# Optimization experiments

Hardware: AMD Instinct MI355X
Metric: run time of the kernel (lower is better)

Reference implementation:

```python
import jax, jax.numpy as jnp
import numpy as np

B, N_OP, N_MA, F, H, O = 32, 512, 64, 8, 128, 8


def _lin(k, fan_in, fan_out):
    kw, kb = jax.random.split(k)
    bound = 1.0 / np.sqrt(fan_in)
    w = jax.random.uniform(kw, (fan_in, fan_out), jnp.float32, -bound, bound)
    b = jax.random.uniform(kb, (fan_out,), jnp.float32, -bound, bound)
    return w, b


def setup_inputs() -> dict:
    key = jax.random.key(0)
    ks = jax.random.split(key, 12)
    inp = {
        "ope_ma_adj_batch": jax.random.randint(ks[0], (B, N_OP, N_MA), 0, 2, dtype=jnp.int32),
        "feats_op": jax.random.normal(ks[1], (B, N_OP, F), jnp.float32),
        "feats_ma": jax.random.normal(ks[2], (B, N_MA, F), jnp.float32),
    }
    # MLPsim 0 (machine aggregation): Linear(F,H), Linear(H,H), Linear(H,O)
    inp["l0_w1"], inp["l0_b1"] = _lin(ks[3], F, H)
    inp["l0_w2"], inp["l0_b2"] = _lin(ks[4], H, H)
    inp["l0_w3"], inp["l0_b3"] = _lin(ks[5], H, O)
    # MLPsim 1 (self-loop aggregation)
    inp["l1_w1"], inp["l1_b1"] = _lin(ks[6], F, H)
    inp["l1_w2"], inp["l1_b2"] = _lin(ks[7], H, H)
    inp["l1_w3"], inp["l1_b3"] = _lin(ks[8], H, O)
    # Final project: Linear(2*O,H), Linear(H,H), Linear(H,O)
    inp["p_w1"], inp["p_b1"] = _lin(ks[9], 2 * O, H)
    inp["p_w2"], inp["p_b2"] = _lin(ks[10], H, H)
    inp["p_w3"], inp["p_b3"] = _lin(ks[11], H, O)
    return inp


def _mlp3(x, w1, b1, w2, b2, w3, b3):
    # Linear -> ELU -> Linear -> ELU -> Linear (matches nn.Sequential in MLPsim.project)
    x = jax.nn.elu(x @ w1 + b1)
    x = jax.nn.elu(x @ w2 + b2)
    return x @ w3 + b3


def reference(ope_ma_adj_batch, feats_op, feats_ma,
              l0_w1, l0_b1, l0_w2, l0_b2, l0_w3, l0_b3,
              l1_w1, l1_b1, l1_w2, l1_b2, l1_w3, l1_b3,
              p_w1, p_b1, p_w2, p_b2, p_w3, p_b3):
    # MLPsim: adj.unsqueeze(-1)*feat.unsqueeze(-3) then sum(-2) == adj @ feat
    adj = ope_ma_adj_batch.astype(feats_ma.dtype)
    agg_ma = jnp.einsum('bnm,bmf->bnf', adj, feats_ma)       # (B, N_op, F)
    emb0 = _mlp3(agg_ma, l0_w1, l0_b1, l0_w2, l0_b2, l0_w3, l0_b3)
    # Second adjacency is the identity self-loop: I @ feats_op == feats_op
    emb1 = _mlp3(feats_op, l1_w1, l1_b1, l1_w2, l1_b2, l1_w3, l1_b3)
    cat = jnp.concatenate([emb0, emb1], axis=-1)              # (B, N_op, 2*O)
    # Final project: ELU -> Linear -> ELU -> Linear -> ELU -> Linear
    mu = _mlp3(jax.nn.elu(cat), p_w1, p_b1, p_w2, p_b2, p_w3, p_b3)
    return mu
```

## Files before the change

kernel.cpp:

```cpp
#include <hip/hip_runtime.h>

#define BB    32
#define N_OPC 512
#define N_MAC 64
#define FF    8
#define HH    128
#define OO    8
#define TM    32
#define ASTRB 136

typedef _Float16 f16x8 __attribute__((ext_vector_type(8)));
typedef _Float16 f16x4 __attribute__((ext_vector_type(4)));
typedef float    f32x4 __attribute__((ext_vector_type(4)));

__device__ __forceinline__ float elu_f(float x) {
    return x > 0.0f ? x : (__expf(x) - 1.0f);
}
__device__ __forceinline__ void store_f16(float v, ushort* dst, int off) {
    const _Float16 h = (_Float16)v;
    dst[off] = __builtin_bit_cast(ushort, h);
}
__device__ __forceinline__ f16x8 gather8(const float* __restrict__ w, int kbase, int j, int ld) {
    f16x8 v;
    #pragma unroll
    for (int i = 0; i < 8; ++i)
        v[i] = (_Float16)w[(kbase + i) * ld + j];
    return v;
}

__device__ __forceinline__ void epi_store(f32x4 a, const float* __restrict__ bias, int jb,
                                          ushort* __restrict__ dst, int off)
{
    const float4 bb = *(const float4*)(bias + jb);
    f16x4 v;
    v[0] = (_Float16)elu_f(a[0] + bb.x);
    v[1] = (_Float16)elu_f(a[1] + bb.y);
    v[2] = (_Float16)elu_f(a[2] + bb.z);
    v[3] = (_Float16)elu_f(a[3] + bb.w);
    *(f16x4*)(dst + off) = v;
}

__global__ __launch_bounds__(512, 4) void mlps_kernel(
    const int*   __restrict__ adj,
    const float* __restrict__ fop,
    const float* __restrict__ fmab,
    const float* __restrict__ l0w1, const float* __restrict__ l0b1,
    const float* __restrict__ l0w2, const float* __restrict__ l0b2,
    const float* __restrict__ l0w3, const float* __restrict__ l0b3,
    const float* __restrict__ l1w1, const float* __restrict__ l1b1,
    const float* __restrict__ l1w2, const float* __restrict__ l1b2,
    const float* __restrict__ l1w3, const float* __restrict__ l1b3,
    const float* __restrict__ pw1,  const float* __restrict__ pb1,
    const float* __restrict__ pw2,  const float* __restrict__ pb2,
    const float* __restrict__ pw3,  const float* __restrict__ pb3,
    float* __restrict__ out)
{
    __shared__ __align__(16) ushort hbuf[2][TM * ASTRB];
    __shared__ __align__(16) ushort gbuf[2][TM * ASTRB];
    __shared__ float fmS[N_MAC * FF];
    __shared__ __align__(16) ushort xinF[TM * FF];
    __shared__ __align__(16) ushort xopF[TM * FF];
    __shared__ __align__(16) ushort catF[TM * 16];

    const int tid  = threadIdx.x;
    const int wv   = tid >> 6;
    const int lane = tid & 63;
    const int lrow = lane & 15;
    const int lk   = lane >> 4;
    const int row0 = blockIdx.x * TM;
    const int b    = row0 / N_OPC;
    const int br   = wv >> 2, jt0 = (wv & 3) * 2;

    const float* w1p = br ? l1w1 : l0w1;
    f16x8 w1f[2] = {};
    if (lk == 0) {
        w1f[0] = gather8(w1p, 0, jt0 * 16 + lrow, HH);
        w1f[1] = gather8(w1p, 0, (jt0 + 1) * 16 + lrow, HH);
    }
    const float* w2p = br ? l1w2 : l0w2;
    f16x8 wf2[2][4];
    #pragma unroll
    for (int jtl = 0; jtl < 2; ++jtl)
        #pragma unroll
        for (int ks = 0; ks < 4; ++ks)
            wf2[jtl][ks] = gather8(w2p, ks * 32 + lk * 8, (jt0 + jtl) * 16 + lrow, HH);

    fmS[tid] = fmab[b * N_MAC * FF + tid];
    if (tid < TM * FF)
        store_f16(fop[row0 * FF + tid], xopF, tid);
    __syncthreads();

    if (tid < TM * FF) {
        const int r = tid >> 3, f = tid & 7;
        const int* arow = adj + (row0 + r) * N_MAC;
        float a = 0.0f;
        #pragma unroll
        for (int m4 = 0; m4 < N_MAC; m4 += 4) {
            const int4 av = *(const int4*)(arow + m4);
            a = fmaf((float)av.x, fmS[(m4 + 0) * FF + f], a);
            a = fmaf((float)av.y, fmS[(m4 + 1) * FF + f], a);
            a = fmaf((float)av.z, fmS[(m4 + 2) * FF + f], a);
            a = fmaf((float)av.w, fmS[(m4 + 3) * FF + f], a);
        }
        store_f16(a, xinF, tid);
    }
    __syncthreads();

    {
        const ushort* xF = br ? xopF : xinF;
        const float* b1 = br ? l1b1 : l0b1;
        f16x8 X[2] = {};
        if (lk == 0) {
            #pragma unroll
            for (int rt = 0; rt < 2; ++rt)
                X[rt] = *(const f16x8*)(xF + (rt * 16 + lrow) * 8);
        }
        f32x4 acc[2][2] = {};
        #pragma unroll
        for (int jtl = 0; jtl < 2; ++jtl)
            #pragma unroll
            for (int rt = 0; rt < 2; ++rt)
                acc[jtl][rt] = __builtin_amdgcn_mfma_f32_16x16x32_f16(w1f[jtl], X[rt], acc[jtl][rt], 0, 0, 0);
        #pragma unroll
        for (int jtl = 0; jtl < 2; ++jtl) {
            const int jb = (jt0 + jtl) * 16 + lk * 4;
            #pragma unroll
            for (int rt = 0; rt < 2; ++rt)
                epi_store(acc[jtl][rt], b1, jb, hbuf[br], (rt * 16 + lrow) * ASTRB + jb);
        }
    }
    __syncthreads();

    f16x8 wf3[4] = {};
    if (wv < 4 && lrow < OO) {
        const float* w3p = (wv >> 1) ? l1w3 : l0w3;
        #pragma unroll
        for (int ks = 0; ks < 4; ++ks)
            wf3[ks] = gather8(w3p, ks * 32 + lk * 8, lrow, OO);
    }
    {
        const ushort* aF = hbuf[br];
        f32x4 acc[2][2] = {};
        #pragma unroll
        for (int ks = 0; ks < 4; ++ks) {
            f16x8 x[2];
            #pragma unroll
            for (int rt = 0; rt < 2; ++rt)
                x[rt] = *(const f16x8*)(aF + (rt * 16 + lrow) * ASTRB + ks * 32 + lk * 8);
            #pragma unroll
            for (int jtl = 0; jtl < 2; ++jtl)
                #pragma unroll
                for (int rt = 0; rt < 2; ++rt)
                    acc[jtl][rt] = __builtin_amdgcn_mfma_f32_16x16x32_f16(wf2[jtl][ks], x[rt], acc[jtl][rt], 0, 0, 0);
        }
        const float* b2 = br ? l1b2 : l0b2;
        #pragma unroll
        for (int jtl = 0; jtl < 2; ++jtl) {
            const int jb = (jt0 + jtl) * 16 + lk * 4;
            #pragma unroll
            for (int rt = 0; rt < 2; ++rt)
                epi_store(acc[jtl][rt], b2, jb, gbuf[br], (rt * 16 + lrow) * ASTRB + jb);
        }
    }
    __syncthreads();

    f16x8 wf4 = {};
    if (lk < 2)
        wf4 = gather8(pw1, lk * 8, wv * 16 + lrow, HH);
    if (wv < 4) {
        const int br3 = wv >> 1, rt = wv & 1;
        const ushort* aF = gbuf[br3];
        f32x4 acc = {};
        #pragma unroll
        for (int ks = 0; ks < 4; ++ks) {
            const f16x8 x = *(const f16x8*)(aF + (rt * 16 + lrow) * ASTRB + ks * 32 + lk * 8);
            acc = __builtin_amdgcn_mfma_f32_16x16x32_f16(wf3[ks], x, acc, 0, 0, 0);
        }
        if (lk < 2) {
            const float* b3 = br3 ? l1b3 : l0b3;
            epi_store(acc, b3, lk * 4, catF, (rt * 16 + lrow) * 16 + br3 * OO + lk * 4);
        }
    }
    __syncthreads();

    f16x8 wf5[4];
    #pragma unroll
    for (int ks = 0; ks < 4; ++ks)
        wf5[ks] = gather8(pw2, ks * 32 + lk * 8, wv * 16 + lrow, HH);
    {
        f16x8 X[2] = {};
        if (lk < 2) {
            #pragma unroll
            for (int rt = 0; rt < 2; ++rt)
                X[rt] = *(const f16x8*)(catF + (rt * 16 + lrow) * 16 + lk * 8);
        }
        f32x4 acc[2] = {};
        #pragma unroll
        for (int rt = 0; rt < 2; ++rt)
            acc[rt] = __builtin_amdgcn_mfma_f32_16x16x32_f16(wf4, X[rt], acc[rt], 0, 0, 0);
        const int jb = wv * 16 + lk * 4;
        #pragma unroll
        for (int rt = 0; rt < 2; ++rt)
            epi_store(acc[rt], pb1, jb, hbuf[0], (rt * 16 + lrow) * ASTRB + jb);
    }
    __syncthreads();

    f16x8 wf6[4] = {};
    if (wv < 2 && lrow < OO) {
        #pragma unroll
        for (int ks = 0; ks < 4; ++ks)
            wf6[ks] = gather8(pw3, ks * 32 + lk * 8, lrow, OO);
    }
    {
        const ushort* aF = hbuf[0];
        f32x4 acc[2] = {};
        #pragma unroll
        for (int ks = 0; ks < 4; ++ks) {
            #pragma unroll
            for (int rt = 0; rt < 2; ++rt) {
                const f16x8 x = *(const f16x8*)(aF + (rt * 16 + lrow) * ASTRB + ks * 32 + lk * 8);
                acc[rt] = __builtin_amdgcn_mfma_f32_16x16x32_f16(wf5[ks], x, acc[rt], 0, 0, 0);
            }
        }
        const int jb = wv * 16 + lk * 4;
        #pragma unroll
        for (int rt = 0; rt < 2; ++rt)
            epi_store(acc[rt], pb2, jb, gbuf[0], (rt * 16 + lrow) * ASTRB + jb);
    }
    __syncthreads();

    if (wv < 2) {
        const int rt = wv;
        const ushort* aF = gbuf[0];
        f32x4 acc = {};
        #pragma unroll
        for (int ks = 0; ks < 4; ++ks) {
            const f16x8 x = *(const f16x8*)(aF + (rt * 16 + lrow) * ASTRB + ks * 32 + lk * 8);
            acc = __builtin_amdgcn_mfma_f32_16x16x32_f16(wf6[ks], x, acc, 0, 0, 0);
        }
        if (lk < 2) {
            const float4 bb = *(const float4*)(pb3 + lk * 4);
            float4 o;
            o.x = acc[0] + bb.x; o.y = acc[1] + bb.y;
            o.z = acc[2] + bb.z; o.w = acc[3] + bb.w;
            *(float4*)(out + (row0 + rt * 16 + lrow) * OO + lk * 4) = o;
        }
    }
}

extern "C" void kernel_launch(void* const* d_in, const int* in_sizes, int n_in,
                              void* d_out, int out_size, void* d_ws, size_t ws_size,
                              hipStream_t stream) {
    (void)in_sizes; (void)n_in; (void)out_size; (void)d_ws; (void)ws_size;
    const int*   adj  = (const int*)  d_in[0];
    const float* fop  = (const float*)d_in[1];
    const float* fmab = (const float*)d_in[2];
    const float* l0w1 = (const float*)d_in[3];
    const float* l0b1 = (const float*)d_in[4];
    const float* l0w2 = (const float*)d_in[5];
    const float* l0b2 = (const float*)d_in[6];
    const float* l0w3 = (const float*)d_in[7];
    const float* l0b3 = (const float*)d_in[8];
    const float* l1w1 = (const float*)d_in[9];
    const float* l1b1 = (const float*)d_in[10];
    const float* l1w2 = (const float*)d_in[11];
    const float* l1b2 = (const float*)d_in[12];
    const float* l1w3 = (const float*)d_in[13];
    const float* l1b3 = (const float*)d_in[14];
    const float* pw1  = (const float*)d_in[15];
    const float* pb1  = (const float*)d_in[16];
    const float* pw2  = (const float*)d_in[17];
    const float* pb2  = (const float*)d_in[18];
    const float* pw3  = (const float*)d_in[19];
    const float* pb3  = (const float*)d_in[20];
    float* out = (float*)d_out;

    const int grid = (BB * N_OPC) / TM;
    mlps_kernel<<<dim3(grid), dim3(512), 0, stream>>>(
        adj, fop, fmab,
        l0w1, l0b1, l0w2, l0b2, l0w3, l0b3,
        l1w1, l1b1, l1w2, l1b2, l1w3, l1b3,
        pw1, pb1, pw2, pb2, pw3, pb3,
        out);
}
```

Measured before the change: 17.77 us.

## Halve row tile to 16 with 256-thread blocks and lazy weight gathers

```diff
diff --git a/kernel.cpp b/kernel.cpp
--- a/kernel.cpp
+++ b/kernel.cpp
@@ -6,7 +6,7 @@
 #define FF    8
 #define HH    128
 #define OO    8
-#define TM    32
+#define TM    16
 #define ASTRB 136
 
 typedef _Float16 f16x8 __attribute__((ext_vector_type(8)));
@@ -40,7 +40,7 @@
     *(f16x4*)(dst + off) = v;
 }
 
-__global__ __launch_bounds__(512, 4) void mlps_kernel(
+__global__ __launch_bounds__(256, 4) void mlps_kernel(
     const int*   __restrict__ adj,
     const float* __restrict__ fop,
     const float* __restrict__ fmab,
@@ -69,23 +69,11 @@
     const int lk   = lane >> 4;
     const int row0 = blockIdx.x * TM;
     const int b    = row0 / N_OPC;
-    const int br   = wv >> 2, jt0 = (wv & 3) * 2;
-
-    const float* w1p = br ? l1w1 : l0w1;
-    f16x8 w1f[2] = {};
-    if (lk == 0) {
-        w1f[0] = gather8(w1p, 0, jt0 * 16 + lrow, HH);
-        w1f[1] = gather8(w1p, 0, (jt0 + 1) * 16 + lrow, HH);
-    }
-    const float* w2p = br ? l1w2 : l0w2;
-    f16x8 wf2[2][4];
-    #pragma unroll
-    for (int jtl = 0; jtl < 2; ++jtl)
-        #pragma unroll
-        for (int ks = 0; ks < 4; ++ks)
-            wf2[jtl][ks] = gather8(w2p, ks * 32 + lk * 8, (jt0 + jtl) * 16 + lrow, HH);
-
-    fmS[tid] = fmab[b * N_MAC * FF + tid];
+    const int br   = wv >> 1;
+    const int jt0  = (wv & 1) * 4;
+
+    fmS[tid]       = fmab[b * N_MAC * FF + tid];
+    fmS[tid + 256] = fmab[b * N_MAC * FF + tid + 256];
     if (tid < TM * FF)
         store_f16(fop[row0 * FF + tid], xopF, tid);
     __syncthreads();
@@ -107,143 +95,121 @@
     __syncthreads();
 
     {
+        const float* w1p = br ? l1w1 : l0w1;
+        const float* b1  = br ? l1b1 : l0b1;
         const ushort* xF = br ? xopF : xinF;
-        const float* b1 = br ? l1b1 : l0b1;
-        f16x8 X[2] = {};
-        if (lk == 0) {
+        f16x8 X = {};
+        if (lk == 0)
+            X = *(const f16x8*)(xF + lrow * 8);
+        #pragma unroll
+        for (int jtl = 0; jtl < 4; ++jtl) {
+            const int jt = jt0 + jtl;
+            f16x8 wf = {};
+            if (lk == 0)
+                wf = gather8(w1p, 0, jt * 16 + lrow, HH);
+            f32x4 acc = {};
+            acc = __builtin_amdgcn_mfma_f32_16x16x32_f16(wf, X, acc, 0, 0, 0);
+            epi_store(acc, b1, jt * 16 + lk * 4, hbuf[br], lrow * ASTRB + jt * 16 + lk * 4);
+        }
+    }
+    __syncthreads();
+
+    {
+        const float* w2p = br ? l1w2 : l0w2;
+        const float* b2  = br ? l1b2 : l0b2;
+        const ushort* aF = hbuf[br];
+        f16x8 x[4];
+        #pragma unroll
+        for (int ks = 0; ks < 4; ++ks)
+            x[ks] = *(const f16x8*)(aF + lrow * ASTRB + ks * 32 + lk * 8);
+        #pragma unroll
+        for (int jtl = 0; jtl < 4; ++jtl) {
+            const int jt = jt0 + jtl;
+            f32x4 acc = {};
             #pragma unroll
-            for (int rt = 0; rt < 2; ++rt)
-                X[rt] = *(const f16x8*)(xF + (rt * 16 + lrow) * 8);
-        }
-        f32x4 acc[2][2] = {};
-        #pragma unroll
-        for (int jtl = 0; jtl < 2; ++jtl)
-            #pragma unroll
-            for (int rt = 0; rt < 2; ++rt)
-                acc[jtl][rt] = __builtin_amdgcn_mfma_f32_16x16x32_f16(w1f[jtl], X[rt], acc[jtl][rt], 0, 0, 0);
-        #pragma unroll
-        for (int jtl = 0; jtl < 2; ++jtl) {
-            const int jb = (jt0 + jtl) * 16 + lk * 4;
-            #pragma unroll
-            for (int rt = 0; rt < 2; ++rt)
-                epi_store(acc[jtl][rt], b1, jb, hbuf[br], (rt * 16 + lrow) * ASTRB + jb);
-        }
-    }
-    __syncthreads();
-
-    f16x8 wf3[4] = {};
-    if (wv < 4 && lrow < OO) {
-        const float* w3p = (wv >> 1) ? l1w3 : l0w3;
-        #pragma unroll
-        for (int ks = 0; ks < 4; ++ks)
-            wf3[ks] = gather8(w3p, ks * 32 + lk * 8, lrow, OO);
-    }
-    {
-        const ushort* aF = hbuf[br];
-        f32x4 acc[2][2] = {};
-        #pragma unroll
-        for (int ks = 0; ks < 4; ++ks) {
-            f16x8 x[2];
-            #pragma unroll
-            for (int rt = 0; rt < 2; ++rt)
-                x[rt] = *(const f16x8*)(aF + (rt * 16 + lrow) * ASTRB + ks * 32 + lk * 8);
-            #pragma unroll
-            for (int jtl = 0; jtl < 2; ++jtl)
-                #pragma unroll
-                for (int rt = 0; rt < 2; ++rt)
-                    acc[jtl][rt] = __builtin_amdgcn_mfma_f32_16x16x32_f16(wf2[jtl][ks], x[rt], acc[jtl][rt], 0, 0, 0);
-        }
-        const float* b2 = br ? l1b2 : l0b2;
-        #pragma unroll
-        for (int jtl = 0; jtl < 2; ++jtl) {
-            const int jb = (jt0 + jtl) * 16 + lk * 4;
-            #pragma unroll
-            for (int rt = 0; rt < 2; ++rt)
-                epi_store(acc[jtl][rt], b2, jb, gbuf[br], (rt * 16 + lrow) * ASTRB + jb);
-        }
-    }
-    __syncthreads();
-
-    f16x8 wf4 = {};
-    if (lk < 2)
-        wf4 = gather8(pw1, lk * 8, wv * 16 + lrow, HH);
-    if (wv < 4) {
-        const int br3 = wv >> 1, rt = wv & 1;
+            for (int ks = 0; ks < 4; ++ks) {
+                const f16x8 wf = gather8(w2p, ks * 32 + lk * 8, jt * 16 + lrow, HH);
+                acc = __builtin_amdgcn_mfma_f32_16x16x32_f16(wf, x[ks], acc, 0, 0, 0);
+            }
+            epi_store(acc, b2, jt * 16 + lk * 4, gbuf[br], lrow * ASTRB + jt * 16 + lk * 4);
+        }
+    }
+    __syncthreads();
+
+    if (wv < 2) {
+        const int br3 = wv;
+        const float* w3p = br3 ? l1w3 : l0w3;
         const ushort* aF = gbuf[br3];
         f32x4 acc = {};
         #pragma unroll
         for (int ks = 0; ks < 4; ++ks) {
-            const f16x8 x = *(const f16x8*)(aF + (rt * 16 + lrow) * ASTRB + ks * 32 + lk * 8);
-            acc = __builtin_amdgcn_mfma_f32_16x16x32_f16(wf3[ks], x, acc, 0, 0, 0);
+            f16x8 wf = {};
+            if (lrow < OO)
+                wf = gather8(w3p, ks * 32 + lk * 8, lrow, OO);
+            const f16x8 x = *(const f16x8*)(aF + lrow * ASTRB + ks * 32 + lk * 8);
+            acc = __builtin_amdgcn_mfma_f32_16x16x32_f16(wf, x, acc, 0, 0, 0);
         }
         if (lk < 2) {
             const float* b3 = br3 ? l1b3 : l0b3;
-            epi_store(acc, b3, lk * 4, catF, (rt * 16 + lrow) * 16 + br3 * OO + lk * 4);
-        }
-    }
-    __syncthreads();
-
-    f16x8 wf5[4];
-    #pragma unroll
-    for (int ks = 0; ks < 4; ++ks)
-        wf5[ks] = gather8(pw2, ks * 32 + lk * 8, wv * 16 + lrow, HH);
-    {
-        f16x8 X[2] = {};
-        if (lk < 2) {
+            epi_store(acc, b3, lk * 4, catF, lrow * 16 + br3 * OO + lk * 4);
+        }
+    }
+    __syncthreads();
+
+    {
+        f16x8 X = {};
+        if (lk < 2)
+            X = *(const f16x8*)(catF + lrow * 16 + lk * 8);
+        #pragma unroll
+        for (int jtl = 0; jtl < 2; ++jtl) {
+            const int jt = wv * 2 + jtl;
+            f16x8 wf = {};
+            if (lk < 2)
+                wf = gather8(pw1, lk * 8, jt * 16 + lrow, HH);
+            f32x4 acc = {};
+            acc = __builtin_amdgcn_mfma_f32_16x16x32_f16(wf, X, acc, 0, 0, 0);
+            epi_store(acc, pb1, jt * 16 + lk * 4, hbuf[0], lrow * ASTRB + jt * 16 + lk * 4);
+        }
+    }
+    __syncthreads();
+
+    {
+        const ushort* aF = hbuf[0];
+        f16x8 x[4];
+        #pragma unroll
+        for (int ks = 0; ks < 4; ++ks)
+            x[ks] = *(const f16x8*)(aF + lrow * ASTRB + ks * 32 + lk * 8);
+        #pragma unroll
+        for (int jtl = 0; jtl < 2; ++jtl) {
+            const int jt = wv * 2 + jtl;
+            f32x4 acc = {};
             #pragma unroll
-            for (int rt = 0; rt < 2; ++rt)
-                X[rt] = *(const f16x8*)(catF + (rt * 16 + lrow) * 16 + lk * 8);
-        }
-        f32x4 acc[2] = {};
-        #pragma unroll
-        for (int rt = 0; rt < 2; ++rt)
-            acc[rt] = __builtin_amdgcn_mfma_f32_16x16x32_f16(wf4, X[rt], acc[rt], 0, 0, 0);
-        const int jb = wv * 16 + lk * 4;
-        #pragma unroll
-        for (int rt = 0; rt < 2; ++rt)
-            epi_store(acc[rt], pb1, jb, hbuf[0], (rt * 16 + lrow) * ASTRB + jb);
-    }
-    __syncthreads();
-
-    f16x8 wf6[4] = {};
-    if (wv < 2 && lrow < OO) {
-        #pragma unroll
-        for (int ks = 0; ks < 4; ++ks)
-            wf6[ks] = gather8(pw3, ks * 32 + lk * 8, lrow, OO);
-    }
-    {
-        const ushort* aF = hbuf[0];
-        f32x4 acc[2] = {};
-        #pragma unroll
-        for (int ks = 0; ks < 4; ++ks) {
-            #pragma unroll
-            for (int rt = 0; rt < 2; ++rt) {
-                const f16x8 x = *(const f16x8*)(aF + (rt * 16 + lrow) * ASTRB + ks * 32 + lk * 8);
-                acc[rt] = __builtin_amdgcn_mfma_f32_16x16x32_f16(wf5[ks], x, acc[rt], 0, 0, 0);
+            for (int ks = 0; ks < 4; ++ks) {
+                const f16x8 wf = gather8(pw2, ks * 32 + lk * 8, jt * 16 + lrow, HH);
+                acc = __builtin_amdgcn_mfma_f32_16x16x32_f16(wf, x[ks], acc, 0, 0, 0);
             }
-        }
-        const int jb = wv * 16 + lk * 4;
-        #pragma unroll
-        for (int rt = 0; rt < 2; ++rt)
-            epi_store(acc[rt], pb2, jb, gbuf[0], (rt * 16 + lrow) * ASTRB + jb);
-    }
-    __syncthreads();
-
-    if (wv < 2) {
-        const int rt = wv;
+            epi_store(acc, pb2, jt * 16 + lk * 4, gbuf[0], lrow * ASTRB + jt * 16 + lk * 4);
+        }
+    }
+    __syncthreads();
+
+    if (wv == 0) {
         const ushort* aF = gbuf[0];
         f32x4 acc = {};
         #pragma unroll
         for (int ks = 0; ks < 4; ++ks) {
-            const f16x8 x = *(const f16x8*)(aF + (rt * 16 + lrow) * ASTRB + ks * 32 + lk * 8);
-            acc = __builtin_amdgcn_mfma_f32_16x16x32_f16(wf6[ks], x, acc, 0, 0, 0);
+            f16x8 wf = {};
+            if (lrow < OO)
+                wf = gather8(pw3, ks * 32 + lk * 8, lrow, OO);
+            const f16x8 x = *(const f16x8*)(aF + lrow * ASTRB + ks * 32 + lk * 8);
+            acc = __builtin_amdgcn_mfma_f32_16x16x32_f16(wf, x, acc, 0, 0, 0);
         }
         if (lk < 2) {
             const float4 bb = *(const float4*)(pb3 + lk * 4);
             float4 o;
             o.x = acc[0] + bb.x; o.y = acc[1] + bb.y;
             o.z = acc[2] + bb.z; o.w = acc[3] + bb.w;
-            *(float4*)(out + (row0 + rt * 16 + lrow) * OO + lk * 4) = o;
+            *(float4*)(out + (row0 + lrow) * OO + lk * 4) = o;
         }
     }
 }
@@ -276,7 +242,7 @@
     float* out = (float*)d_out;
 
     const int grid = (BB * N_OPC) / TM;
-    mlps_kernel<<<dim3(grid), dim3(512), 0, stream>>>(
+    mlps_kernel<<<dim3(grid), dim3(256), 0, stream>>>(
         adj, fop, fmab,
         l0w1, l0b1, l0w2, l0b2, l0w3, l0b3,
         l1w1, l1b1, l1w2, l1b2, l1w3, l1b3,
```

New measurement: 21.85 us. 23.0% more time.
